# Kernel tuning notes

Measured on AMD Instinct MI355X. Metric: run time of the kernel, lower is better.

Reference implementation:

```python
import jax, jax.numpy as jnp
import numpy as np

B, M, S, A = 256, 256, 32, 33
NH, NOUT = 3, 100
F_IN = 2 * S + 2          # 66, GAT input features
ALPHA = 0.01              # leaky-relu slope
LN_EPS = 1e-5


def setup_inputs() -> dict:
    key = jax.random.key(0)
    ks = jax.random.split(key, 13)
    obs_dim = 5 * M + 2 + 2 * M * S
    obs = jax.random.normal(ks[0], (B, obs_dim), jnp.float32)
    adj = jax.random.randint(ks[1], (M, M), 0, 2).astype(jnp.int32)
    u_gumbel = jax.random.uniform(ks[2], (B, M, A), jnp.float32)
    W_gat = jax.random.normal(ks[3], (NH, F_IN, NOUT), jnp.float32) * 0.1
    a_gat = jax.random.normal(ks[4], (NH, 2 * NOUT), jnp.float32) * 0.1
    ln_w = jax.random.normal(ks[5], (NH * NOUT,), jnp.float32) * 0.5
    ln_b = jnp.zeros((NH * NOUT,), jnp.float32)
    W1 = jax.random.normal(ks[6], (3 * M + 2, 100), jnp.float32) * 0.05
    b1 = jax.random.normal(ks[7], (100,), jnp.float32) * 0.7
    d2_in = 100 + NH * M * NOUT
    W2 = jax.random.normal(ks[8], (d2_in, 128), jnp.float32) * 0.005
    b2 = jax.random.normal(ks[9], (128,), jnp.float32) * 0.7
    Wout = jax.random.normal(ks[10], (M, 128, A), jnp.float32) * 0.1
    bout = jax.random.normal(ks[11], (M, A), jnp.float32) * 0.7
    return dict(obs=obs, adj=adj, u_gumbel=u_gumbel, W_gat=W_gat, a_gat=a_gat,
                ln_w=ln_w, ln_b=ln_b, W1=W1, b1=b1, W2=W2, b2=b2,
                Wout=Wout, bout=bout)


def _actor_fwd(obs, u_gumbel, W_gat, a_gat, ln_w, ln_b, W1, b1, W2, b2, Wout, bout, adj):
    # --- split obs per Actor.forward slicing ---
    server_state = obs[:, :3 * M + 2]                       # [B, 3m+2]
    mcs_res = obs[:, 3 * M + 2:4 * M + 2].reshape(B, M, 1)
    mcs_ins = obs[:, 4 * M + 2:5 * M + 2].reshape(B, M, 1)
    base = 5 * M + 2
    resp = obs[:, base:base + M * S].reshape(B, M, S)
    insp = obs[:, base + M * S:].reshape(B, M, S)
    feat = jnp.concatenate([mcs_res, mcs_ins, resp, insp], axis=-1)  # [B,M,2s+2]

    # --- GAT layer (eval mode: dropouts are identity) ---
    Wh = jnp.einsum('bmf,hfo->hbmo', feat, W_gat)           # [H,B,M,O]
    # e[b,i,j] = leakyrelu(a1 . Wh_i + a2 . Wh_j)  (same math as the
    # original O(N^2,2f) repeat/cat, expressed without materializing it)
    e1 = jnp.einsum('hbmo,ho->hbm', Wh, a_gat[:, :NOUT])
    e2 = jnp.einsum('hbmo,ho->hbm', Wh, a_gat[:, NOUT:])
    e = jax.nn.leaky_relu(e1[..., :, None] + e2[..., None, :], ALPHA)  # [H,B,M,M]
    e = jnp.where(adj > 0, e, jnp.float32(-9e15))
    att = jax.nn.softmax(e, axis=-2)                        # torch softmax(dim=1)
    h_prime = jax.nn.elu(jnp.einsum('hbij,hbjo->hbio', att, Wh))
    feats = jnp.moveaxis(h_prime, 0, 2).reshape(B, M, NH * NOUT)  # head concat
    mu = jnp.mean(feats, axis=-1, keepdims=True)
    var = jnp.var(feats, axis=-1, keepdims=True)
    gat_out = (feats - mu) * jax.lax.rsqrt(var + LN_EPS) * ln_w + ln_b
    gat_out = jax.nn.elu(gat_out)                           # GAT.forward elu_
    mcs_gat = gat_out.reshape(B, -1)                        # [B, 3*m*100]

    # --- dense heads ---
    server_feat = jax.nn.relu(jax.nn.elu(server_state @ W1 + b1))
    hidden = jax.nn.relu(jax.nn.elu(
        jnp.concatenate([server_feat, mcs_gat], axis=-1) @ W2 + b2))  # [B,128]

    # per-mcs heads, vectorized: logits[b,m,a]
    logits = jnp.tanh(jax.nn.elu(jnp.einsum('bh,mha->bma', hidden, Wout) + bout))

    # gumbel-softmax (tau=1, hard=True, straight-through)
    u = jnp.clip(u_gumbel, 1e-10, 1.0 - 1e-10)
    g = -jnp.log(-jnp.log(u))
    y_soft = jax.nn.softmax(logits + g, axis=-1)
    y_hard = jax.nn.one_hot(jnp.argmax(y_soft, axis=-1), A, dtype=y_soft.dtype)
    actions = y_hard + y_soft - jax.lax.stop_gradient(y_soft)
    return actions.reshape(B, M * A)


def reference(obs, adj, u_gumbel, W_gat, a_gat, ln_w, ln_b, W1, b1, W2, b2, Wout, bout):
    return _actor_fwd(obs, u_gumbel, W_gat, a_gat, ln_w, ln_b, W1, b1, W2, b2, Wout, bout, adj)
```

## Files before the change

### kernel.cpp

```cpp
#include <hip/hip_runtime.h>
#include <math.h>

constexpr int B    = 256;
constexpr int M    = 256;
constexpr int A    = 33;
constexpr int NH   = 3;
constexpr int NO   = 100;
constexpr int FIN  = 66;
constexpr int OBSD = 17666;
constexpr int D1   = 770;
constexpr int D2G  = 76800;

__device__ __forceinline__ float lrelu(float x) { return x > 0.f ? x : 0.01f * x; }
__device__ __forceinline__ float eluf(float x)  { return x > 0.f ? x : expm1f(x); }

__global__ __launch_bounds__(256) void k_adjmask(const int* __restrict__ adj,
                                                 unsigned* __restrict__ adjm) {
  int w = blockIdx.x * 256 + threadIdx.x;
  if (w >= M * 8) return;
  int i = w >> 3, wd = w & 7;
  const int* row = adj + i * M + wd * 32;
  unsigned mval = 0;
  #pragma unroll
  for (int bit = 0; bit < 32; ++bit) mval |= (row[bit] > 0 ? 1u : 0u) << bit;
  adjm[w] = mval;
}

__global__ __launch_bounds__(256) void k_wh(const float* __restrict__ obs,
                                            const float* __restrict__ Wg,
                                            const float* __restrict__ ag,
                                            const unsigned* __restrict__ adjm,
                                            float* __restrict__ Wh,
                                            float* __restrict__ e1,
                                            float* __restrict__ e2,
                                            float* __restrict__ cmax,
                                            float* __restrict__ csum) {
  int b = blockIdx.x, h = blockIdx.y;
  int t = threadIdx.x;
  int to = t >> 4;
  int tm = t & 15;
  __shared__ float smem_w[66 * 104 + 32];
  __shared__ float featT[66 * 132];
  __shared__ float a1s[128], a2s[128];
  __shared__ float e1a[256], e2a[256];
  __shared__ unsigned ams[M * 8];
  const float* ob = obs + (size_t)b * OBSD;

  for (int idx = t; idx < 66 * 104 + 32; idx += 256) {
    float v = 0.f;
    if (idx < 66 * 104) {
      int f = idx / 104, o = idx % 104;
      if (o < NO) v = Wg[((size_t)h * FIN + f) * NO + o];
    }
    smem_w[idx] = v;
  }
  if (t < 128) {
    a1s[t] = (t < NO) ? ag[h * 200 + t] : 0.f;
    a2s[t] = (t < NO) ? ag[h * 200 + NO + t] : 0.f;
  }
  for (int w = t; w < M * 8; w += 256) ams[w] = adjm[w];

  size_t basee = ((size_t)h * B + b) * M;

  for (int tile = 0; tile < 2; ++tile) {
    int m0 = tile * 128;
    if (t < 128)       featT[t]               = ob[770  + m0 + t];
    else               featT[132 + (t - 128)] = ob[1026 + m0 + (t - 128)];
    for (int idx = t; idx < 128 * 32; idx += 256) {
      int m = idx >> 5, s = idx & 31;
      featT[(2  + s) * 132 + m] = ob[1282 + (size_t)(m0 + m) * 32 + s];
      featT[(34 + s) * 132 + m] = ob[9474 + (size_t)(m0 + m) * 32 + s];
    }
    __syncthreads();

    float acc[8][8];
    #pragma unroll
    for (int q = 0; q < 8; ++q)
      #pragma unroll
      for (int p = 0; p < 8; ++p) acc[q][p] = 0.f;

    for (int f = 0; f < 66; ++f) {
      const float* fr = featT + f * 132;
      const float* wr = smem_w + f * 104 + to * 8;
      float4 fa = *(const float4*)(fr + tm * 4);
      float4 fb = *(const float4*)(fr + 64 + tm * 4);
      float4 wa = *(const float4*)wr;
      float4 wb = *(const float4*)(wr + 4);
      float fm[8] = {fa.x, fa.y, fa.z, fa.w, fb.x, fb.y, fb.z, fb.w};
      float wv[8] = {wa.x, wa.y, wa.z, wa.w, wb.x, wb.y, wb.z, wb.w};
      #pragma unroll
      for (int q = 0; q < 8; ++q)
        #pragma unroll
        for (int p = 0; p < 8; ++p) acc[q][p] += fm[q] * wv[p];
    }
    __syncthreads();

    float* e1p = featT;
    float* e2p = featT + 128 * 18;
    #pragma unroll
    for (int q = 0; q < 8; ++q) {
      int ml = (q < 4) ? (tm * 4 + q) : (64 + tm * 4 + q - 4);
      float p1 = 0.f, p2 = 0.f;
      #pragma unroll
      for (int p = 0; p < 8; ++p) {
        float av = acc[q][p];
        p1 += av * a1s[to * 8 + p];
        p2 += av * a2s[to * 8 + p];
      }
      e1p[ml * 18 + to] = p1;
      e2p[ml * 18 + to] = p2;
    }

    #pragma unroll
    for (int q = 0; q < 8; ++q) {
      int ml = (q < 4) ? (tm * 4 + q) : (64 + tm * 4 + q - 4);
      int m = m0 + ml;
      float* wp = Wh + (basee + m) * NO + to * 8;
      if (to <= 12) *(float4*)wp       = make_float4(acc[q][0], acc[q][1], acc[q][2], acc[q][3]);
      if (to <= 11) *(float4*)(wp + 4) = make_float4(acc[q][4], acc[q][5], acc[q][6], acc[q][7]);
    }
    __syncthreads();

    if (t < 128) {
      float s1 = 0.f, s2 = 0.f;
      #pragma unroll
      for (int u = 0; u < 16; ++u) {
        s1 += e1p[t * 18 + u];
        s2 += e2p[t * 18 + u];
      }
      e1[basee + m0 + t] = s1;
      e2[basee + m0 + t] = s2;
      e1a[m0 + t] = s1;
      e2a[m0 + t] = s2;
    }
    __syncthreads();
  }

  {
    float e2j = e2a[t];
    int jw = t >> 5;
    unsigned jb = 1u << (t & 31);
    float mx = -INFINITY;
    #pragma unroll 8
    for (int i = 0; i < M; ++i) {
      float v = (ams[i * 8 + jw] & jb) ? lrelu(e1a[i] + e2j) : -9e15f;
      mx = fmaxf(mx, v);
    }
    float sm = 0.f;
    #pragma unroll 8
    for (int i = 0; i < M; ++i) {
      float v = (ams[i * 8 + jw] & jb) ? lrelu(e1a[i] + e2j) : -9e15f;
      sm += expf(v - mx);
    }
    cmax[basee + t] = mx;
    csum[basee + t] = sm;
  }
}

__global__ __launch_bounds__(256) void k_attn(const float* __restrict__ Wh,
                                              const float* __restrict__ e1,
                                              const float* __restrict__ e2,
                                              const float* __restrict__ cmax,
                                              const float* __restrict__ csum,
                                              const unsigned* __restrict__ adjm,
                                              float* __restrict__ feats) {
  int b = blockIdx.x, h = blockIdx.y, ih = blockIdx.z;
  int t = threadIdx.x;
  int to = t & 15, ti = t >> 4;
  int i0 = ih * 128;
  __shared__ float WhC[32 * 128];
  __shared__ float attT[32 * 132];
  __shared__ float e1s[128];
  __shared__ float e2s[256], cms[256], csr[256];
  size_t base = ((size_t)h * B + b) * M;

  if (t < 128) e1s[t] = e1[base + i0 + t];
  e2s[t] = e2[base + t];
  cms[t] = cmax[base + t];
  csr[t] = 1.0f / csum[base + t];

  float acc[8][8];
  #pragma unroll
  for (int q = 0; q < 8; ++q)
    #pragma unroll
    for (int p = 0; p < 8; ++p) acc[q][p] = 0.f;

  const float* WhG = Wh + base * NO;
  int jp = t >> 3;
  int ib = t & 7;

  for (int c = 0; c < 8; ++c) {
    __syncthreads();
    for (int idx = t; idx < 32 * 128; idx += 256) {
      int r = idx >> 7, o = idx & 127;
      WhC[idx] = (o < NO) ? WhG[(size_t)(c * 32 + r) * NO + o] : 0.f;
    }
    {
      int jg = c * 32 + jp;
      float e2j = e2s[jg], cmj = cms[jg], rsj = csr[jg];
      unsigned wbit = 1u << jp;
      const unsigned* aw = adjm + (size_t)(i0 + ib) * 8 + c;
      const float* ep = e1s + ib;
      float* ap = attT + jp * 132 + ib;
      #pragma unroll
      for (int rr = 0; rr < 16; ++rr) {
        float v = (aw[rr * 64] & wbit) ? lrelu(ep[rr * 8] + e2j) : -9e15f;
        ap[rr * 8] = expf(v - cmj) * rsj;
      }
    }
    __syncthreads();
    for (int j = 0; j < 32; ++j) {
      const float4* a4 = (const float4*)(attT + j * 132 + ti * 8);
      float4 aa = a4[0], ab = a4[1];
      float4 wa = *(const float4*)(WhC + j * 128 + to * 4);
      float4 wb = *(const float4*)(WhC + j * 128 + 64 + to * 4);
      float av[8] = {aa.x, aa.y, aa.z, aa.w, ab.x, ab.y, ab.z, ab.w};
      float wv[8] = {wa.x, wa.y, wa.z, wa.w, wb.x, wb.y, wb.z, wb.w};
      #pragma unroll
      for (int q = 0; q < 8; ++q)
        #pragma unroll
        for (int p = 0; p < 8; ++p) acc[q][p] += av[q] * wv[p];
    }
  }

  #pragma unroll
  for (int q = 0; q < 8; ++q) {
    int i = i0 + ti * 8 + q;
    float* fp = feats + ((size_t)b * M + i) * 300 + h * NO;
    *(float4*)(fp + to * 4) =
        make_float4(eluf(acc[q][0]), eluf(acc[q][1]), eluf(acc[q][2]), eluf(acc[q][3]));
    if (to < 9)
      *(float4*)(fp + 64 + to * 4) =
          make_float4(eluf(acc[q][4]), eluf(acc[q][5]), eluf(acc[q][6]), eluf(acc[q][7]));
  }
}

__global__ __launch_bounds__(256) void k_lnstats(const float* __restrict__ g,
                                                 float* __restrict__ mu_out,
                                                 float* __restrict__ rs_out) {
  int gid = blockIdx.x * 256 + threadIdx.x;
  int wid = gid >> 6, lane = gid & 63;
  const float* row = g + (size_t)wid * 300;
  float v[5];
  float s = 0.f;
  #pragma unroll
  for (int j = 0; j < 5; ++j) {
    int i = j * 64 + lane;
    v[j] = (i < 300) ? row[i] : 0.f;
    s += v[j];
  }
  #pragma unroll
  for (int d = 1; d < 64; d <<= 1) s += __shfl_xor(s, d);
  float mu = s * (1.f / 300.f);
  float ss = 0.f;
  #pragma unroll
  for (int j = 0; j < 5; ++j) {
    int i = j * 64 + lane;
    float dd = (i < 300) ? (v[j] - mu) : 0.f;
    ss += dd * dd;
  }
  #pragma unroll
  for (int d = 1; d < 64; d <<= 1) ss += __shfl_xor(ss, d);
  if (lane == 0) {
    mu_out[wid] = mu;
    rs_out[wid] = 1.0f / sqrtf(ss * (1.f / 300.f) + 1e-5f);
  }
}

__global__ __launch_bounds__(256) void k_gemm2(const float* __restrict__ gat,
                                               const float* __restrict__ mu,
                                               const float* __restrict__ rs,
                                               const float* __restrict__ lw,
                                               const float* __restrict__ lb,
                                               const float* __restrict__ W2,
                                               float* __restrict__ pre) {
  int bt = blockIdx.x, dc = blockIdx.y;
  int t = threadIdx.x;
  int k = t & 127, g2 = t >> 7;
  __shared__ float gt[16 * 124];
  int b0 = bt * 16, d0 = dc * 1200;
  float acc[8];
  #pragma unroll
  for (int r = 0; r < 8; ++r) acc[r] = 0.f;
  for (int ds0 = 0; ds0 < 1200; ds0 += 120) {
    int dsg = d0 + ds0;
    __syncthreads();
    for (int idx = t; idx < 16 * 120; idx += 256) {
      int rr = idx / 120, cc = idx - rr * 120;
      int gidx = dsg + cc;
      int brow = b0 + rr;
      int mrow = gidx / 300;
      int d    = gidx - mrow * 300;
      int lrow = brow * M + mrow;
      float x = gat[(size_t)brow * D2G + gidx];
      float val = (x - mu[lrow]) * rs[lrow] * lw[d] + lb[d];
      gt[rr * 124 + cc] = eluf(val);
    }
    __syncthreads();
    const float* w2p = W2 + (size_t)(100 + dsg) * 128 + k;
    for (int c4 = 0; c4 < 30; ++c4) {
      float w0  = w2p[(size_t)(c4 * 4 + 0) * 128];
      float w1  = w2p[(size_t)(c4 * 4 + 1) * 128];
      float w2v = w2p[(size_t)(c4 * 4 + 2) * 128];
      float w3  = w2p[(size_t)(c4 * 4 + 3) * 128];
      #pragma unroll
      for (int r = 0; r < 8; ++r) {
        float4 gv = *(const float4*)(gt + (g2 * 8 + r) * 124 + c4 * 4);
        acc[r] += gv.x * w0 + gv.y * w1 + gv.z * w2v + gv.w * w3;
      }
    }
  }
  #pragma unroll
  for (int r = 0; r < 8; ++r)
    pre[((size_t)dc * B + b0 + g2 * 8 + r) * 128 + k] = acc[r];
}

__global__ __launch_bounds__(256) void k_hid(const float* __restrict__ pre,
                                             const float* __restrict__ obs,
                                             const float* __restrict__ W1,
                                             const float* __restrict__ b1,
                                             const float* __restrict__ W2,
                                             const float* __restrict__ b2,
                                             float* __restrict__ hid,
                                             float* __restrict__ hidT) {
  int b = blockIdx.x, t = threadIdx.x;
  int k = t & 127, p = t >> 7;
  __shared__ float ssrv[D1];
  __shared__ float sfs[128];
  __shared__ float red[256];
  const float* ob = obs + (size_t)b * OBSD;
  for (int i = t; i < D1; i += 256) ssrv[i] = ob[i];
  __syncthreads();
  float acc = 0.f;
  if (k < NO) {
    int f0 = p * 385;
    #pragma unroll 8
    for (int f = f0; f < f0 + 385; ++f) acc += ssrv[f] * W1[(size_t)f * NO + k];
  }
  red[t] = acc;
  __syncthreads();
  if (t < 128 && k < NO) {
    float v = red[t] + red[t + 128] + b1[k];
    sfs[k] = fmaxf(eluf(v), 0.f);
  }
  __syncthreads();
  float s = 0.f;
  #pragma unroll 4
  for (int dc = p * 32; dc < p * 32 + 32; ++dc)
    s += pre[((size_t)dc * B + b) * 128 + k];
  #pragma unroll 4
  for (int f = p * 50; f < p * 50 + 50; ++f)
    s += sfs[f] * W2[(size_t)f * 128 + k];
  __syncthreads();
  red[t] = s;
  __syncthreads();
  if (t < 128) {
    float v = red[t] + red[t + 128] + b2[k];
    v = fmaxf(eluf(v), 0.f);
    hid[(size_t)b * 128 + k] = v;
    hidT[(size_t)k * B + b]  = v;
  }
}

__global__ __launch_bounds__(256) void k_out(const float* __restrict__ hidT,
                                             const float* __restrict__ Wout,
                                             const float* __restrict__ bout,
                                             const float* __restrict__ ug,
                                             float* __restrict__ out) {
  int m = blockIdx.x, b = threadIdx.x;
  __shared__ float wo[128 * 36];
  for (int idx = b; idx < 128 * 36; idx += 256) {
    int kk = idx / 36, a = idx % 36;
    wo[idx] = (a < A) ? Wout[(size_t)m * 128 * A + kk * A + a] : 0.f;
  }
  __syncthreads();
  float l[36];
  #pragma unroll
  for (int a = 0; a < 36; ++a) l[a] = (a < A) ? bout[m * A + a] : 0.f;
  for (int kk = 0; kk < 128; ++kk) {
    float hv = hidT[(size_t)kk * B + b];
    const float4* w4 = (const float4*)(wo + kk * 36);
    #pragma unroll
    for (int q = 0; q < 9; ++q) {
      float4 wv = w4[q];
      l[4*q+0] += hv * wv.x;
      l[4*q+1] += hv * wv.y;
      l[4*q+2] += hv * wv.z;
      l[4*q+3] += hv * wv.w;
    }
  }
  const float* ugp = ug + ((size_t)b * M + m) * A;
  float mx = -INFINITY;
  int amx = 0;
  #pragma unroll
  for (int a = 0; a < A; ++a) {
    float th = tanhf(eluf(l[a]));
    float u = ugp[a];
    u = fminf(fmaxf(u, 1e-10f), 1.0f - 1e-10f);
    float gb = -logf(-logf(u));
    float z = th + gb;
    l[a] = z;
    if (z > mx) { mx = z; amx = a; }
  }
  float sm = 0.f;
  #pragma unroll
  for (int a = 0; a < A; ++a) { float e = expf(l[a] - mx); l[a] = e; sm += e; }
  float* op = out + ((size_t)b * M + m) * A;
  #pragma unroll
  for (int a = 0; a < A; ++a) {
    float ys = l[a] / sm;
    float yh = (a == amx) ? 1.0f : 0.0f;
    op[a] = (yh + ys) - ys;
  }
}

extern "C" void kernel_launch(void* const* d_in, const int* in_sizes, int n_in,
                              void* d_out, int out_size, void* d_ws, size_t ws_size,
                              hipStream_t stream) {
  const float* obs  = (const float*)d_in[0];
  const int*   adj  = (const int*)  d_in[1];
  const float* ug   = (const float*)d_in[2];
  const float* Wg   = (const float*)d_in[3];
  const float* ag   = (const float*)d_in[4];
  const float* lw   = (const float*)d_in[5];
  const float* lb   = (const float*)d_in[6];
  const float* W1   = (const float*)d_in[7];
  const float* b1   = (const float*)d_in[8];
  const float* W2   = (const float*)d_in[9];
  const float* b2   = (const float*)d_in[10];
  const float* Wout = (const float*)d_in[11];
  const float* bout = (const float*)d_in[12];
  float* out = (float*)d_out;

  float* ws = (float*)d_ws;
  size_t off = 0;
  float* Wh    = ws + off; off += (size_t)NH * B * M * NO;
  float* feats = ws + off; off += (size_t)B * M * 300;
  float* e1    = ws + off; off += (size_t)NH * B * M;
  float* e2    = ws + off; off += (size_t)NH * B * M;
  float* cmx   = ws + off; off += (size_t)NH * B * M;
  float* csm   = ws + off; off += (size_t)NH * B * M;
  float* pre   = ws + off; off += (size_t)64 * B * 128;
  float* hid   = ws + off; off += (size_t)B * 128;
  float* hidT  = ws + off; off += (size_t)B * 128;
  float* muA   = ws + off; off += (size_t)B * M;
  float* rsA   = ws + off; off += (size_t)B * M;
  unsigned* adjm = (unsigned*)(ws + off);

  k_adjmask <<<dim3(8),         256, 0, stream>>>(adj, adjm);
  k_wh      <<<dim3(B, NH),     256, 0, stream>>>(obs, Wg, ag, adjm, Wh, e1, e2, cmx, csm);
  k_attn    <<<dim3(B, NH, 2),  256, 0, stream>>>(Wh, e1, e2, cmx, csm, adjm, feats);
  k_lnstats <<<dim3(B * M / 4), 256, 0, stream>>>(feats, muA, rsA);
  k_gemm2   <<<dim3(16, 64),    256, 0, stream>>>(feats, muA, rsA, lw, lb, W2, pre);
  k_hid     <<<dim3(B),         256, 0, stream>>>(pre, obs, W1, b1, W2, b2, hid, hidT);
  k_out     <<<dim3(M),         256, 0, stream>>>(hidT, Wout, bout, ug, out);
}
```

Baseline: 777.0 us.

## Fuse LayerNorm stats into gemm2, prefetch Wh tiles in attn, split heads

After: 846.8 us. 9.0% more time.

```diff
diff --git a/kernel.cpp b/kernel.cpp
--- a/kernel.cpp
+++ b/kernel.cpp
@@ -79,19 +79,21 @@
       #pragma unroll
       for (int p = 0; p < 8; ++p) acc[q][p] = 0.f;
 
+    const float* frP = featT;
+    const float* wrP = smem_w + to * 8;
     for (int f = 0; f < 66; ++f) {
-      const float* fr = featT + f * 132;
-      const float* wr = smem_w + f * 104 + to * 8;
-      float4 fa = *(const float4*)(fr + tm * 4);
-      float4 fb = *(const float4*)(fr + 64 + tm * 4);
-      float4 wa = *(const float4*)wr;
-      float4 wb = *(const float4*)(wr + 4);
+      float4 fa = *(const float4*)(frP + tm * 4);
+      float4 fb = *(const float4*)(frP + 64 + tm * 4);
+      float4 wa = *(const float4*)wrP;
+      float4 wb = *(const float4*)(wrP + 4);
       float fm[8] = {fa.x, fa.y, fa.z, fa.w, fb.x, fb.y, fb.z, fb.w};
       float wv[8] = {wa.x, wa.y, wa.z, wa.w, wb.x, wb.y, wb.z, wb.w};
       #pragma unroll
       for (int q = 0; q < 8; ++q)
         #pragma unroll
-        for (int p = 0; p < 8; ++p) acc[q][p] += fm[q] * wv[p];
+        for (int p = 0; p < 8; ++p) acc[q][p] = fmaf(fm[q], wv[p], acc[q][p]);
+      frP += 132;
+      wrP += 104;
     }
     __syncthreads();
 
@@ -163,8 +165,9 @@
                                               const float* __restrict__ cmax,
                                               const float* __restrict__ csum,
                                               const unsigned* __restrict__ adjm,
-                                              float* __restrict__ feats) {
-  int b = blockIdx.x, h = blockIdx.y, ih = blockIdx.z;
+                                              float* __restrict__ feats,
+                                              int h) {
+  int b = blockIdx.x, ih = blockIdx.y;
   int t = threadIdx.x;
   int to = t & 15, ti = t >> 4;
   int i0 = ih * 128;
@@ -188,13 +191,25 @@
   const float* WhG = Wh + base * NO;
   int jp = t >> 3;
   int ib = t & 7;
+  int pr_r[4], pr_o4[4];
+  #pragma unroll
+  for (int u = 0; u < 4; ++u) {
+    int idx4 = t + 256 * u;
+    pr_r[u]  = idx4 >> 5;
+    pr_o4[u] = idx4 & 31;
+  }
+  float4 pf[4];
+  #pragma unroll
+  for (int u = 0; u < 4; ++u)
+    pf[u] = (pr_o4[u] < 25)
+          ? *(const float4*)(WhG + (size_t)pr_r[u] * NO + pr_o4[u] * 4)
+          : make_float4(0.f, 0.f, 0.f, 0.f);
 
   for (int c = 0; c < 8; ++c) {
     __syncthreads();
-    for (int idx = t; idx < 32 * 128; idx += 256) {
-      int r = idx >> 7, o = idx & 127;
-      WhC[idx] = (o < NO) ? WhG[(size_t)(c * 32 + r) * NO + o] : 0.f;
-    }
+    #pragma unroll
+    for (int u = 0; u < 4; ++u)
+      *(float4*)(WhC + pr_r[u] * 128 + pr_o4[u] * 4) = pf[u];
     {
       int jg = c * 32 + jp;
       float e2j = e2s[jg], cmj = cms[jg], rsj = csr[jg];
@@ -208,18 +223,32 @@
         ap[rr * 8] = expf(v - cmj) * rsj;
       }
     }
-    __syncthreads();
+    if (c < 7) {
+      const float* WhN = WhG + (size_t)(c + 1) * 32 * NO;
+      #pragma unroll
+      for (int u = 0; u < 4; ++u)
+        pf[u] = (pr_o4[u] < 25)
+              ? *(const float4*)(WhN + (size_t)pr_r[u] * NO + pr_o4[u] * 4)
+              : make_float4(0.f, 0.f, 0.f, 0.f);
+    }
+    __syncthreads();
+    const float* aP  = attT + ti * 8;
+    const float* wP0 = WhC + to * 4;
+    const float* wP1 = WhC + 64 + to * 4;
     for (int j = 0; j < 32; ++j) {
-      const float4* a4 = (const float4*)(attT + j * 132 + ti * 8);
-      float4 aa = a4[0], ab = a4[1];
-      float4 wa = *(const float4*)(WhC + j * 128 + to * 4);
-      float4 wb = *(const float4*)(WhC + j * 128 + 64 + to * 4);
+      float4 aa = *(const float4*)aP;
+      float4 ab = *(const float4*)(aP + 4);
+      float4 wa = *(const float4*)wP0;
+      float4 wb = *(const float4*)wP1;
       float av[8] = {aa.x, aa.y, aa.z, aa.w, ab.x, ab.y, ab.z, ab.w};
       float wv[8] = {wa.x, wa.y, wa.z, wa.w, wb.x, wb.y, wb.z, wb.w};
       #pragma unroll
       for (int q = 0; q < 8; ++q)
         #pragma unroll
-        for (int p = 0; p < 8; ++p) acc[q][p] += av[q] * wv[p];
+        for (int p = 0; p < 8; ++p) acc[q][p] = fmaf(av[q], wv[p], acc[q][p]);
+      aP  += 132;
+      wP0 += 128;
+      wP1 += 128;
     }
   }
 
@@ -235,41 +264,7 @@
   }
 }
 
-__global__ __launch_bounds__(256) void k_lnstats(const float* __restrict__ g,
-                                                 float* __restrict__ mu_out,
-                                                 float* __restrict__ rs_out) {
-  int gid = blockIdx.x * 256 + threadIdx.x;
-  int wid = gid >> 6, lane = gid & 63;
-  const float* row = g + (size_t)wid * 300;
-  float v[5];
-  float s = 0.f;
-  #pragma unroll
-  for (int j = 0; j < 5; ++j) {
-    int i = j * 64 + lane;
-    v[j] = (i < 300) ? row[i] : 0.f;
-    s += v[j];
-  }
-  #pragma unroll
-  for (int d = 1; d < 64; d <<= 1) s += __shfl_xor(s, d);
-  float mu = s * (1.f / 300.f);
-  float ss = 0.f;
-  #pragma unroll
-  for (int j = 0; j < 5; ++j) {
-    int i = j * 64 + lane;
-    float dd = (i < 300) ? (v[j] - mu) : 0.f;
-    ss += dd * dd;
-  }
-  #pragma unroll
-  for (int d = 1; d < 64; d <<= 1) ss += __shfl_xor(ss, d);
-  if (lane == 0) {
-    mu_out[wid] = mu;
-    rs_out[wid] = 1.0f / sqrtf(ss * (1.f / 300.f) + 1e-5f);
-  }
-}
-
 __global__ __launch_bounds__(256) void k_gemm2(const float* __restrict__ gat,
-                                               const float* __restrict__ mu,
-                                               const float* __restrict__ rs,
                                                const float* __restrict__ lw,
                                                const float* __restrict__ lb,
                                                const float* __restrict__ W2,
@@ -278,7 +273,34 @@
   int t = threadIdx.x;
   int k = t & 127, g2 = t >> 7;
   __shared__ float gt[16 * 124];
+  __shared__ float mu_s[64], rs_s[64];
+  __shared__ float part[64][4];
   int b0 = bt * 16, d0 = dc * 1200;
+
+  {
+    int row = t >> 2, seg = t & 3;
+    int brow = b0 + (row >> 2);
+    int mloc = row & 3;
+    const float* rp = gat + (size_t)brow * D2G + (size_t)(dc * 4 + mloc) * 300 + seg * 75;
+    float s = 0.f;
+    #pragma unroll 5
+    for (int i = 0; i < 75; ++i) s += rp[i];
+    part[row][seg] = s;
+    __syncthreads();
+    if (t < 64)
+      mu_s[t] = (part[t][0] + part[t][1] + part[t][2] + part[t][3]) * (1.f / 300.f);
+    __syncthreads();
+    float mu = mu_s[row];
+    float ss = 0.f;
+    #pragma unroll 5
+    for (int i = 0; i < 75; ++i) { float d = rp[i] - mu; ss += d * d; }
+    part[row][seg] = ss;
+    __syncthreads();
+    if (t < 64)
+      rs_s[t] = 1.0f / sqrtf((part[t][0] + part[t][1] + part[t][2] + part[t][3]) * (1.f / 300.f) + 1e-5f);
+    __syncthreads();
+  }
+
   float acc[8];
   #pragma unroll
   for (int r = 0; r < 8; ++r) acc[r] = 0.f;
@@ -291,9 +313,9 @@
       int brow = b0 + rr;
       int mrow = gidx / 300;
       int d    = gidx - mrow * 300;
-      int lrow = brow * M + mrow;
+      int lr   = rr * 4 + (mrow - dc * 4);
       float x = gat[(size_t)brow * D2G + gidx];
-      float val = (x - mu[lrow]) * rs[lrow] * lw[d] + lb[d];
+      float val = (x - mu_s[lr]) * rs_s[lr] * lw[d] + lb[d];
       gt[rr * 124 + cc] = eluf(val);
     }
     __syncthreads();
@@ -306,7 +328,10 @@
       #pragma unroll
       for (int r = 0; r < 8; ++r) {
         float4 gv = *(const float4*)(gt + (g2 * 8 + r) * 124 + c4 * 4);
-        acc[r] += gv.x * w0 + gv.y * w1 + gv.z * w2v + gv.w * w3;
+        acc[r] = fmaf(gv.x, w0, acc[r]);
+        acc[r] = fmaf(gv.y, w1, acc[r]);
+        acc[r] = fmaf(gv.z, w2v, acc[r]);
+        acc[r] = fmaf(gv.w, w3, acc[r]);
       }
     }
   }
@@ -383,10 +408,10 @@
     #pragma unroll
     for (int q = 0; q < 9; ++q) {
       float4 wv = w4[q];
-      l[4*q+0] += hv * wv.x;
-      l[4*q+1] += hv * wv.y;
-      l[4*q+2] += hv * wv.z;
-      l[4*q+3] += hv * wv.w;
+      l[4*q+0] = fmaf(hv, wv.x, l[4*q+0]);
+      l[4*q+1] = fmaf(hv, wv.y, l[4*q+1]);
+      l[4*q+2] = fmaf(hv, wv.z, l[4*q+2]);
+      l[4*q+3] = fmaf(hv, wv.w, l[4*q+3]);
     }
   }
   const float* ugp = ug + ((size_t)b * M + m) * A;
@@ -443,15 +468,14 @@
   float* pre   = ws + off; off += (size_t)64 * B * 128;
   float* hid   = ws + off; off += (size_t)B * 128;
   float* hidT  = ws + off; off += (size_t)B * 128;
-  float* muA   = ws + off; off += (size_t)B * M;
-  float* rsA   = ws + off; off += (size_t)B * M;
   unsigned* adjm = (unsigned*)(ws + off);
 
-  k_adjmask <<<dim3(8),         256, 0, stream>>>(adj, adjm);
-  k_wh      <<<dim3(B, NH),     256, 0, stream>>>(obs, Wg, ag, adjm, Wh, e1, e2, cmx, csm);
-  k_attn    <<<dim3(B, NH, 2),  256, 0, stream>>>(Wh, e1, e2, cmx, csm, adjm, feats);
-  k_lnstats <<<dim3(B * M / 4), 256, 0, stream>>>(feats, muA, rsA);
-  k_gemm2   <<<dim3(16, 64),    256, 0, stream>>>(feats, muA, rsA, lw, lb, W2, pre);
-  k_hid     <<<dim3(B),         256, 0, stream>>>(pre, obs, W1, b1, W2, b2, hid, hidT);
-  k_out     <<<dim3(M),         256, 0, stream>>>(hidT, Wout, bout, ug, out);
-}
+  k_adjmask <<<dim3(8),       256, 0, stream>>>(adj, adjm);
+  k_wh      <<<dim3(B, NH),   256, 0, stream>>>(obs, Wg, ag, adjm, Wh, e1, e2, cmx, csm);
+  k_attn    <<<dim3(B, 2),    256, 0, stream>>>(Wh, e1, e2, cmx, csm, adjm, feats, 0);
+  k_attn    <<<dim3(B, 2),    256, 0, stream>>>(Wh, e1, e2, cmx, csm, adjm, feats, 1);
+  k_attn    <<<dim3(B, 2),    256, 0, stream>>>(Wh, e1, e2, cmx, csm, adjm, feats, 2);
+  k_gemm2   <<<dim3(16, 64),  256, 0, stream>>>(feats, lw, lb, W2, pre);
+  k_hid     <<<dim3(B),       256, 0, stream>>>(pre, obs, W1, b1, W2, b2, hid, hidT);
+  k_out     <<<dim3(M),       256, 0, stream>>>(hidT, Wout, bout, ug, out);
+}
```
